# Kernel optimization log

Measured on AMD Instinct MI355X. Metric: run time of the kernel, lower is better.

The kernel has to match this reference:

```python
import jax, jax.numpy as jnp
import numpy as np

EPS = 1e-6


def box2corners(box):
    # box (N,5): x, y, w, h, alpha -> corners (N,4,2), CCW starting at (+w/2,+h/2)
    x, y, w, h, a = (box[:, i] for i in range(5))
    dx = jnp.array([0.5, -0.5, -0.5, 0.5], dtype=box.dtype)
    dy = jnp.array([0.5, 0.5, -0.5, -0.5], dtype=box.dtype)
    cx = dx[None, :] * w[:, None]
    cy = dy[None, :] * h[:, None]
    cos, sin = jnp.cos(a)[:, None], jnp.sin(a)[:, None]
    rx = cx * cos - cy * sin + x[:, None]
    ry = cx * sin + cy * cos + y[:, None]
    return jnp.stack([rx, ry], axis=-1)


def box_intersections(c1, c2):
    # Pairwise intersections of the 4 edges of box1 with the 4 edges of box2.
    # c1, c2: (N,4,2) -> points (N,16,2), valid mask (N,16)
    l1 = jnp.concatenate([c1, jnp.roll(c1, -1, axis=1)], axis=-1)[:, :, None, :]  # (N,4,1,4)
    l2 = jnp.concatenate([c2, jnp.roll(c2, -1, axis=1)], axis=-1)[:, None, :, :]  # (N,1,4,4)
    x1, y1, x2, y2 = (l1[..., i] for i in range(4))
    x3, y3, x4, y4 = (l2[..., i] for i in range(4))
    den = (x2 - x1) * (y4 - y3) - (y2 - y1) * (x4 - x3)
    den_safe = jnp.where(den == 0, 1.0, den)
    t = ((x3 - x1) * (y4 - y3) - (y3 - y1) * (x4 - x3)) / den_safe
    u = ((x3 - x1) * (y2 - y1) - (y3 - y1) * (x2 - x1)) / den_safe
    mask = (den != 0) & (t > 0.0) & (t < 1.0) & (u > 0.0) & (u < 1.0)
    px = x1 + t * (x2 - x1)
    py = y1 + t * (y2 - y1)
    pts = jnp.stack([px, py], axis=-1) * mask[..., None]
    N = c1.shape[0]
    return pts.reshape(N, 16, 2), mask.reshape(N, 16)


def corners_in_box(c1, c2):
    # Which corners of box1 lie inside box2, via projection onto box2 edges. (N,4) bool
    a = c2[:, 0:1]
    ab = c2[:, 1:2] - a
    ad = c2[:, 3:4] - a
    am = c1 - a  # (N,4,2)
    p_ab = (am * ab).sum(-1) / (ab * ab).sum(-1)
    p_ad = (am * ad).sum(-1) / (ad * ad).sum(-1)
    tol = 1e-6
    return (p_ab > -tol) & (p_ab < 1 + tol) & (p_ad > -tol) & (p_ad < 1 + tol)


def sorted_poly_area(pts, mask):
    # Sort valid vertices CCW around the valid-vertex mean, pad invalid slots with the
    # first sorted vertex (degenerate edges contribute 0), then shoelace area.
    # pts (N,M,2), mask (N,M) bool -> area (N,)
    maskf = mask.astype(pts.dtype)
    num = jnp.maximum(maskf.sum(-1, keepdims=True), 1.0)  # avoid /0 for empty polygons
    mean = (pts * maskf[..., None]).sum(1, keepdims=True) / num[..., None]
    centered = pts - mean
    ang = jnp.arctan2(centered[..., 1], centered[..., 0])
    ang = jnp.where(mask, ang, 1e9)  # invalid vertices sort last
    order = jnp.argsort(ang, axis=-1)
    sp = jnp.take_along_axis(pts, order[..., None], axis=1)
    sm = jnp.take_along_axis(mask, order, axis=1)
    sp = jnp.where(sm[..., None], sp, sp[:, 0:1])  # pad with first (valid) vertex
    nxt = jnp.roll(sp, -1, axis=1)
    cross = sp[..., 0] * nxt[..., 1] - sp[..., 1] * nxt[..., 0]
    return jnp.abs(cross.sum(-1)) * 0.5


def intersection_area(c1, c2):
    # Differentiable convex-polygon intersection area (Rotated_IoU style):
    # candidate vertices = corners of each box inside the other + edge intersections.
    ipts, imask = box_intersections(c1, c2)
    m1 = corners_in_box(c1, c2)
    m2 = corners_in_box(c2, c1)
    pts = jnp.concatenate([c1, c2, ipts], axis=1)    # (N,24,2)
    mask = jnp.concatenate([m1, m2, imask], axis=1)  # (N,24)
    return sorted_poly_area(pts, mask)


def poly_giou_loss(pred, target, weight):
    areas1 = pred[:, 2] * pred[:, 3]
    areas2 = target[:, 2] * target[:, 3]
    c1 = box2corners(pred)
    c2 = box2corners(target)
    overlap = intersection_area(c1, c2)
    union = areas1 + areas2 - overlap + EPS
    ious = jnp.maximum(overlap / union, EPS)
    # poly_enclose: all 8 corners, all valid
    all_pts = jnp.concatenate([c1, c2], axis=1)  # (N,8,2)
    enclose = sorted_poly_area(all_pts, jnp.ones(all_pts.shape[:2], bool))
    gious = ious - (enclose - union) / enclose
    loss = 1.0 - gious
    # weighted_loss with reduction='mean', avg_factor=None, loss_weight=1.0
    return (loss * weight).mean()


def setup_inputs() -> dict:
    key = jax.random.key(0)
    k1, k2, k3, k4, k5 = jax.random.split(key, 5)
    N = 500000
    xy = jax.random.uniform(k1, (N, 2), dtype=jnp.float32) * 100.0
    wh = jax.random.uniform(k2, (N, 2), dtype=jnp.float32) * 10.0 + 1.0
    ang = (jax.random.uniform(k3, (N, 1), dtype=jnp.float32) - 0.5) * np.float32(np.pi)
    pred = jnp.concatenate([xy, wh, ang], axis=-1)
    noise = jax.random.normal(k4, (N, 5), dtype=jnp.float32) * jnp.array(
        [1.0, 1.0, 0.5, 0.5, 0.1], dtype=jnp.float32)
    target = pred + noise
    target = target.at[:, 2:4].set(jnp.maximum(target[:, 2:4], 0.5))
    weight = jax.random.uniform(k5, (N,), dtype=jnp.float32)
    return {"pred": pred, "target": target, "weight": weight}


def reference(pred, target, weight):
    return poly_giou_loss(pred, target, weight)
```

## Files before the change

kernel.cpp:

```cpp
#include <hip/hip_runtime.h>
#include <math.h>

#define BLOCK 128
#define NS 8

__device__ __forceinline__ float fast_rcp(float x) {
    return __builtin_amdgcn_rcpf(x);
}

__device__ __forceinline__ float pseudo_angle(float x, float y) {
    float d = fabsf(x) + fabsf(y);
    float p = (d == 0.f) ? 1.f : x * fast_rcp(d);
    return (y < 0.f) ? (p - 1.f) : (1.f - p);
}

__launch_bounds__(BLOCK)
__global__ void giou_kernel(const float* __restrict__ pred,
                            const float* __restrict__ target,
                            const float* __restrict__ weight,
                            float* __restrict__ partials, int N) {
    __shared__ float2 bufA[NS][BLOCK];
    __shared__ float2 bufB[NS][BLOCK];

    int tid = threadIdx.x;
    long gi = (long)blockIdx.x * BLOCK + tid;
    int i = (gi < (long)N) ? (int)gi : (N - 1);

    float p[5], q[5];
#pragma unroll
    for (int j = 0; j < 5; ++j) p[j] = pred[i * 5 + j];
#pragma unroll
    for (int j = 0; j < 5; ++j) q[j] = target[i * 5 + j];
    float wgt = weight[i];

    const float dxs[4] = {0.5f, -0.5f, -0.5f, 0.5f};
    const float dys[4] = {0.5f, 0.5f, -0.5f, -0.5f};
    float c1x[4], c1y[4], c2x[4], c2y[4];
    {
        float sn, cs;
        sincosf(p[4], &sn, &cs);
#pragma unroll
        for (int j = 0; j < 4; ++j) {
            float cx = dxs[j] * p[2], cy = dys[j] * p[3];
            c1x[j] = cx * cs - cy * sn + p[0];
            c1y[j] = cx * sn + cy * cs + p[1];
        }
        sincosf(q[4], &sn, &cs);
#pragma unroll
        for (int j = 0; j < 4; ++j) {
            float cx = dxs[j] * q[2], cy = dys[j] * q[3];
            c2x[j] = cx * cs - cy * sn + q[0];
            c2y[j] = cx * sn + cy * cs + q[1];
        }
    }

    int m1 = 0;
    {
        float e0x = c2x[1] - c2x[0], e0y = c2y[1] - c2y[0];
        float e2x = c2x[3] - c2x[2], e2y = c2y[3] - c2y[2];
        float sA[4], sB[4];
#pragma unroll
        for (int j = 0; j < 4; ++j) {
            sA[j] = e0x * (c1y[j] - c2y[0]) - e0y * (c1x[j] - c2x[0]);
            sB[j] = e2x * (c1y[j] - c2y[2]) - e2y * (c1x[j] - c2x[2]);
        }
#pragma unroll
        for (int e = 0; e < 4; ++e) {
            int en = (e + 1) & 3;
            float cx = c1x[e], cy = c1y[e];
            float dx = c1x[en] - cx, dy = c1y[en] - cy;
            float sac = sA[e], san = sA[en];
            float sbc = sB[e], sbn = sB[en];
            bool inC = (sac >= 0.f) && (sbc >= 0.f);
            bool cA = (sac >= 0.f) != (san >= 0.f);
            bool cB = (sbc >= 0.f) != (sbn >= 0.f);
            float tA = sac * fast_rcp(sac - san);
            float tB = sbc * fast_rcp(sbc - sbn);
            float XAx = fmaf(tA, dx, cx), XAy = fmaf(tA, dy, cy);
            float XBx = fmaf(tB, dx, cx), XBy = fmaf(tB, dy, cy);
            if (inC) { bufA[m1][tid] = make_float2(cx, cy); m1++; }
            bool fA = cA && (!cB || (tA <= tB));
            float X1x = fA ? XAx : XBx, X1y = fA ? XAy : XBy;
            float X2x = fA ? XBx : XAx, X2y = fA ? XBy : XAy;
            if (cA || cB) { bufA[m1][tid] = make_float2(X1x, X1y); m1++; }
            if (cA && cB) { bufA[m1][tid] = make_float2(X2x, X2y); m1++; }
        }
    }
    int n1 = (m1 < 6) ? m1 : 6;

    int m2 = 0;
    {
        float e1x = c2x[2] - c2x[1], e1y = c2y[2] - c2y[1];
        float e3x = c2x[0] - c2x[3], e3y = c2y[0] - c2y[3];
        float vx[6], vy[6], s1[6], s3[6];
#pragma unroll
        for (int j = 0; j < 6; ++j) {
            float2 v = bufA[j][tid];
            vx[j] = v.x; vy[j] = v.y;
            s1[j] = e1x * (v.y - c2y[1]) - e1y * (v.x - c2x[1]);
            s3[j] = e3x * (v.y - c2y[3]) - e3y * (v.x - c2x[3]);
        }
#pragma unroll
        for (int e = 0; e < 6; ++e) {
            bool act = (e < n1);
            bool last = (e == n1 - 1);
            int en = (e + 1 < 6) ? e + 1 : 0;
            float nx = last ? vx[0] : vx[en];
            float ny = last ? vy[0] : vy[en];
            float san = last ? s1[0] : s1[en];
            float sbn = last ? s3[0] : s3[en];
            float cx = vx[e], cy = vy[e];
            float dx = nx - cx, dy = ny - cy;
            float sac = s1[e], sbc = s3[e];
            bool inC = (sac >= 0.f) && (sbc >= 0.f);
            bool cA = (sac >= 0.f) != (san >= 0.f);
            bool cB = (sbc >= 0.f) != (sbn >= 0.f);
            float tA = sac * fast_rcp(sac - san);
            float tB = sbc * fast_rcp(sbc - sbn);
            float XAx = fmaf(tA, dx, cx), XAy = fmaf(tA, dy, cy);
            float XBx = fmaf(tB, dx, cx), XBy = fmaf(tB, dy, cy);
            if (act && inC && m2 < NS) { bufB[m2][tid] = make_float2(cx, cy); m2++; }
            bool fA = cA && (!cB || (tA <= tB));
            float X1x = fA ? XAx : XBx, X1y = fA ? XAy : XBy;
            float X2x = fA ? XBx : XAx, X2y = fA ? XBy : XAy;
            if (act && (cA || cB) && m2 < NS) { bufB[m2][tid] = make_float2(X1x, X1y); m2++; }
            if (act && cA && cB && m2 < NS) { bufB[m2][tid] = make_float2(X2x, X2y); m2++; }
        }
    }
    int n2 = (m2 < NS) ? m2 : NS;

    float overlap;
    {
        float fx[8], fy[8];
#pragma unroll
        for (int k = 0; k < 8; ++k) {
            float2 v = bufB[k][tid];
            fx[k] = v.x; fy[k] = v.y;
        }
#pragma unroll
        for (int k = 1; k < 8; ++k) {
            bool u = (k < n2);
            fx[k] = u ? fx[k] : fx[0];
            fy[k] = u ? fy[k] : fy[0];
        }
        float acc = 0.f;
#pragma unroll
        for (int k = 0; k < 8; ++k) {
            int kn = (k + 1) & 7;
            acc += fx[k] * fy[kn] - fy[k] * fx[kn];
        }
        overlap = 0.5f * fabsf(acc);
        overlap = (n2 >= 3) ? overlap : 0.f;
    }

    float enc;
    {
        float px[8], py[8];
#pragma unroll
        for (int j = 0; j < 4; ++j) {
            px[j] = c1x[j];     py[j] = c1y[j];
            px[4 + j] = c2x[j]; py[4 + j] = c2y[j];
        }
        float ex = 0.f, ey = 0.f;
#pragma unroll
        for (int j = 0; j < 8; ++j) { ex += px[j]; ey += py[j]; }
        float mx = ex * 0.125f, my = ey * 0.125f;
        float ang[8];
#pragma unroll
        for (int j = 0; j < 8; ++j) ang[j] = pseudo_angle(px[j] - mx, py[j] - my);
#pragma unroll
        for (int j = 0; j < 8; ++j) {
            int r = 0;
#pragma unroll
            for (int k = 0; k < 8; ++k) {
                if (k < j)      r += (ang[k] <= ang[j]) ? 1 : 0;
                else if (k > j) r += (ang[k] <  ang[j]) ? 1 : 0;
            }
            bufA[r][tid] = make_float2(px[j], py[j]);
        }
        float sx0[8], sy0[8];
#pragma unroll
        for (int k = 0; k < 8; ++k) {
            float2 v = bufA[k][tid];
            sx0[k] = v.x; sy0[k] = v.y;
        }
        float acc = 0.f;
#pragma unroll
        for (int k = 0; k < 8; ++k) {
            int kn = (k + 1) & 7;
            acc += sx0[k] * sy0[kn] - sy0[k] * sx0[kn];
        }
        enc = 0.5f * fabsf(acc);
    }

    float area1 = p[2] * p[3];
    float area2 = q[2] * q[3];
    float uni = area1 + area2 - overlap + 1e-6f;
    float iou = fmaxf(overlap / uni, 1e-6f);
    float giou = iou - (enc - uni) / enc;
    float loss = (1.f - giou) * wgt;
    if (gi >= (long)N) loss = 0.f;

#pragma unroll
    for (int off = 32; off > 0; off >>= 1)
        loss += __shfl_down(loss, off, 64);
    if ((tid & 63) == 0)
        partials[blockIdx.x * (BLOCK / 64) + (tid >> 6)] = loss;
}

__launch_bounds__(256)
__global__ void reduce_kernel(const float* __restrict__ partials,
                              float* __restrict__ out, int nparts, float scale) {
    __shared__ float acc[4];
    int tid = threadIdx.x;
    float s = 0.f;
    for (int j = tid; j < nparts; j += 256) s += partials[j];
#pragma unroll
    for (int off = 32; off > 0; off >>= 1)
        s += __shfl_down(s, off, 64);
    if ((tid & 63) == 0) acc[tid >> 6] = s;
    __syncthreads();
    if (tid == 0) out[0] = (acc[0] + acc[1] + acc[2] + acc[3]) * scale;
}

extern "C" void kernel_launch(void* const* d_in, const int* in_sizes, int n_in,
                              void* d_out, int out_size, void* d_ws, size_t ws_size,
                              hipStream_t stream) {
    const float* pred   = (const float*)d_in[0];
    const float* target = (const float*)d_in[1];
    const float* weight = (const float*)d_in[2];
    float* out = (float*)d_out;
    float* ws  = (float*)d_ws;
    int N = in_sizes[0] / 5;

    int nblocks = (N + BLOCK - 1) / BLOCK;
    int nparts = nblocks * (BLOCK / 64);
    giou_kernel<<<nblocks, BLOCK, 0, stream>>>(pred, target, weight, ws, N);
    reduce_kernel<<<1, 256, 0, stream>>>(ws, out, nparts, 1.0f / (float)N);
}
```

Baseline: 89.07 us.

## Clip in target's local frame with streaming shoelace, drop LDS clip buffers

The prediction box is transformed into the target box's local frame, where the target is axis-aligned, so Sutherland-Hodgman clipping reduces to comparisons against ±hw and ±hh. Intersection vertices are fed straight into a running shoelace accumulator instead of being written to shared-memory buffers, which removes the bufB array and the intermediate LDS traffic. Accurate sincosf is replaced with the hardware sin/cos builtins, and the final reduction uses 1024 threads instead of 256. The risks are reduced precision from the approximate trig and numerical differences from the changed-frame geometry.

```diff
diff --git a/kernel.cpp b/kernel.cpp
--- a/kernel.cpp
+++ b/kernel.cpp
@@ -2,16 +2,55 @@
 #include <math.h>
 
 #define BLOCK 128
-#define NS 8
 
 __device__ __forceinline__ float fast_rcp(float x) {
     return __builtin_amdgcn_rcpf(x);
+}
+__device__ __forceinline__ float fsin(float x) {
+    return __builtin_amdgcn_sinf(x * 0.15915494309189535f);
+}
+__device__ __forceinline__ float fcos(float x) {
+    return __builtin_amdgcn_cosf(x * 0.15915494309189535f);
 }
 
 __device__ __forceinline__ float pseudo_angle(float x, float y) {
     float d = fabsf(x) + fabsf(y);
     float p = (d == 0.f) ? 1.f : x * fast_rcp(d);
     return (y < 0.f) ? (p - 1.f) : (1.f - p);
+}
+
+struct Shoe {
+    float sfx, sfy, spx, spy, acc;
+    bool have;
+};
+
+__device__ __forceinline__ void emit(Shoe& s, bool c, float X, float Y) {
+    float cr = s.spx * Y - s.spy * X;
+    s.acc += (c && s.have) ? cr : 0.f;
+    s.sfx = (c && !s.have) ? X : s.sfx;
+    s.sfy = (c && !s.have) ? Y : s.sfy;
+    s.spx = c ? X : s.spx;
+    s.spy = c ? Y : s.spy;
+    s.have = s.have || c;
+}
+
+__device__ __forceinline__ void edge_clip_y(Shoe& s, bool en, float ax, float ay,
+                                            float bx, float by, float hh) {
+    bool inA = en && (ay <= hh) && (ay >= -hh);
+    bool cA = en && ((ay > hh) != (by > hh));
+    bool cB = en && ((ay < -hh) != (by < -hh));
+    float dxe = bx - ax, dye = by - ay;
+    float rd = fast_rcp(dye);
+    float tA = (hh - ay) * rd;
+    float tB = (-hh - ay) * rd;
+    float xA = fmaf(tA, dxe, ax);
+    float xB = fmaf(tB, dxe, ax);
+    bool fA = cA && (!cB || (tA <= tB));
+    float e1x = fA ? xA : xB, e1y = fA ? hh : -hh;
+    float e2x = fA ? xB : xA, e2y = fA ? -hh : hh;
+    emit(s, inA, ax, ay);
+    emit(s, cA || cB, e1x, e1y);
+    emit(s, cA && cB, e2x, e2y);
 }
 
 __launch_bounds__(BLOCK)
@@ -19,8 +58,7 @@
                             const float* __restrict__ target,
                             const float* __restrict__ weight,
                             float* __restrict__ partials, int N) {
-    __shared__ float2 bufA[NS][BLOCK];
-    __shared__ float2 bufB[NS][BLOCK];
+    __shared__ float2 bufA[8][BLOCK];
 
     int tid = threadIdx.x;
     long gi = (long)blockIdx.x * BLOCK + tid;
@@ -33,141 +71,83 @@
     for (int j = 0; j < 5; ++j) q[j] = target[i * 5 + j];
     float wgt = weight[i];
 
-    const float dxs[4] = {0.5f, -0.5f, -0.5f, 0.5f};
-    const float dys[4] = {0.5f, 0.5f, -0.5f, -0.5f};
-    float c1x[4], c1y[4], c2x[4], c2y[4];
-    {
-        float sn, cs;
-        sincosf(p[4], &sn, &cs);
-#pragma unroll
-        for (int j = 0; j < 4; ++j) {
-            float cx = dxs[j] * p[2], cy = dys[j] * p[3];
-            c1x[j] = cx * cs - cy * sn + p[0];
-            c1y[j] = cx * sn + cy * cs + p[1];
-        }
-        sincosf(q[4], &sn, &cs);
-#pragma unroll
-        for (int j = 0; j < 4; ++j) {
-            float cx = dxs[j] * q[2], cy = dys[j] * q[3];
-            c2x[j] = cx * cs - cy * sn + q[0];
-            c2y[j] = cx * sn + cy * cs + q[1];
-        }
-    }
-
-    int m1 = 0;
-    {
-        float e0x = c2x[1] - c2x[0], e0y = c2y[1] - c2y[0];
-        float e2x = c2x[3] - c2x[2], e2y = c2y[3] - c2y[2];
-        float sA[4], sB[4];
-#pragma unroll
-        for (int j = 0; j < 4; ++j) {
-            sA[j] = e0x * (c1y[j] - c2y[0]) - e0y * (c1x[j] - c2x[0]);
-            sB[j] = e2x * (c1y[j] - c2y[2]) - e2y * (c1x[j] - c2x[2]);
-        }
-#pragma unroll
-        for (int e = 0; e < 4; ++e) {
-            int en = (e + 1) & 3;
-            float cx = c1x[e], cy = c1y[e];
-            float dx = c1x[en] - cx, dy = c1y[en] - cy;
-            float sac = sA[e], san = sA[en];
-            float sbc = sB[e], sbn = sB[en];
-            bool inC = (sac >= 0.f) && (sbc >= 0.f);
-            bool cA = (sac >= 0.f) != (san >= 0.f);
-            bool cB = (sbc >= 0.f) != (sbn >= 0.f);
-            float tA = sac * fast_rcp(sac - san);
-            float tB = sbc * fast_rcp(sbc - sbn);
-            float XAx = fmaf(tA, dx, cx), XAy = fmaf(tA, dy, cy);
-            float XBx = fmaf(tB, dx, cx), XBy = fmaf(tB, dy, cy);
-            if (inC) { bufA[m1][tid] = make_float2(cx, cy); m1++; }
-            bool fA = cA && (!cB || (tA <= tB));
-            float X1x = fA ? XAx : XBx, X1y = fA ? XAy : XBy;
-            float X2x = fA ? XBx : XAx, X2y = fA ? XBy : XAy;
-            if (cA || cB) { bufA[m1][tid] = make_float2(X1x, X1y); m1++; }
-            if (cA && cB) { bufA[m1][tid] = make_float2(X2x, X2y); m1++; }
-        }
-    }
-    int n1 = (m1 < 6) ? m1 : 6;
-
-    int m2 = 0;
-    {
-        float e1x = c2x[2] - c2x[1], e1y = c2y[2] - c2y[1];
-        float e3x = c2x[0] - c2x[3], e3y = c2y[0] - c2y[3];
-        float vx[6], vy[6], s1[6], s3[6];
-#pragma unroll
-        for (int j = 0; j < 6; ++j) {
-            float2 v = bufA[j][tid];
-            vx[j] = v.x; vy[j] = v.y;
-            s1[j] = e1x * (v.y - c2y[1]) - e1y * (v.x - c2x[1]);
-            s3[j] = e3x * (v.y - c2y[3]) - e3y * (v.x - c2x[3]);
-        }
-#pragma unroll
-        for (int e = 0; e < 6; ++e) {
-            bool act = (e < n1);
-            bool last = (e == n1 - 1);
-            int en = (e + 1 < 6) ? e + 1 : 0;
-            float nx = last ? vx[0] : vx[en];
-            float ny = last ? vy[0] : vy[en];
-            float san = last ? s1[0] : s1[en];
-            float sbn = last ? s3[0] : s3[en];
-            float cx = vx[e], cy = vy[e];
-            float dx = nx - cx, dy = ny - cy;
-            float sac = s1[e], sbc = s3[e];
-            bool inC = (sac >= 0.f) && (sbc >= 0.f);
-            bool cA = (sac >= 0.f) != (san >= 0.f);
-            bool cB = (sbc >= 0.f) != (sbn >= 0.f);
-            float tA = sac * fast_rcp(sac - san);
-            float tB = sbc * fast_rcp(sbc - sbn);
-            float XAx = fmaf(tA, dx, cx), XAy = fmaf(tA, dy, cy);
-            float XBx = fmaf(tB, dx, cx), XBy = fmaf(tB, dy, cy);
-            if (act && inC && m2 < NS) { bufB[m2][tid] = make_float2(cx, cy); m2++; }
-            bool fA = cA && (!cB || (tA <= tB));
-            float X1x = fA ? XAx : XBx, X1y = fA ? XAy : XBy;
-            float X2x = fA ? XBx : XAx, X2y = fA ? XBy : XAy;
-            if (act && (cA || cB) && m2 < NS) { bufB[m2][tid] = make_float2(X1x, X1y); m2++; }
-            if (act && cA && cB && m2 < NS) { bufB[m2][tid] = make_float2(X2x, X2y); m2++; }
-        }
-    }
-    int n2 = (m2 < NS) ? m2 : NS;
-
-    float overlap;
-    {
-        float fx[8], fy[8];
-#pragma unroll
-        for (int k = 0; k < 8; ++k) {
-            float2 v = bufB[k][tid];
-            fx[k] = v.x; fy[k] = v.y;
-        }
-#pragma unroll
-        for (int k = 1; k < 8; ++k) {
-            bool u = (k < n2);
-            fx[k] = u ? fx[k] : fx[0];
-            fy[k] = u ? fy[k] : fy[0];
-        }
-        float acc = 0.f;
-#pragma unroll
-        for (int k = 0; k < 8; ++k) {
-            int kn = (k + 1) & 7;
-            acc += fx[k] * fy[kn] - fy[k] * fx[kn];
-        }
-        overlap = 0.5f * fabsf(acc);
-        overlap = (n2 >= 3) ? overlap : 0.f;
-    }
+    float cq = fcos(q[4]), sq = fsin(q[4]);
+    float dang = p[4] - q[4];
+    float cd = fcos(dang), sd = fsin(dang);
+    float hw = 0.5f * q[2], hh = 0.5f * q[3];
+    float dxc = p[0] - q[0], dyc = p[1] - q[1];
+    float tx = dxc * cq + dyc * sq;
+    float ty = -dxc * sq + dyc * cq;
+    float ax_ = 0.5f * p[2] * cd, ay_ = 0.5f * p[2] * sd;
+    float bx_ = -0.5f * p[3] * sd, by_ = 0.5f * p[3] * cd;
+
+    float qx[4], qy[4];
+    qx[0] = tx + ax_ + bx_; qy[0] = ty + ay_ + by_;
+    qx[1] = tx - ax_ + bx_; qy[1] = ty - ay_ + by_;
+    qx[2] = tx - ax_ - bx_; qy[2] = ty - ay_ - by_;
+    qx[3] = tx + ax_ - bx_; qy[3] = ty + ay_ - by_;
+
+    float sxk[8], syk[8];
+    bool sv[8];
+#pragma unroll
+    for (int e = 0; e < 4; ++e) {
+        int en = (e + 1) & 3;
+        float xc = qx[e], yc = qy[e], xn = qx[en], yn = qy[en];
+        float dxe = xn - xc, dye = yn - yc;
+        bool inC = (xc <= hw) && (xc >= -hw);
+        bool cA = (xc > hw) != (xn > hw);
+        bool cB = (xc < -hw) != (xn < -hw);
+        float rd = fast_rcp(dxe);
+        float tA = (hw - xc) * rd;
+        float tB = (-hw - xc) * rd;
+        float yA = fmaf(tA, dye, yc);
+        float yB = fmaf(tB, dye, yc);
+        bool fA = cA && (!cB || (tA <= tB));
+        float X1x = fA ? hw : -hw, X1y = fA ? yA : yB;
+        float X2x = fA ? -hw : hw, X2y = fA ? yB : yA;
+        sxk[2 * e]     = inC ? xc : X1x;
+        syk[2 * e]     = inC ? yc : X1y;
+        sv[2 * e]      = inC || cA || cB;
+        sxk[2 * e + 1] = inC ? X1x : X2x;
+        syk[2 * e + 1] = inC ? X1y : X2y;
+        sv[2 * e + 1]  = inC ? (cA || cB) : (cA && cB);
+    }
+
+    Shoe sh; sh.sfx = sh.sfy = sh.spx = sh.spy = sh.acc = 0.f; sh.have = false;
+    bool have_p = false;
+    float pfx = 0.f, pfy = 0.f, pvx = 0.f, pvy = 0.f;
+#pragma unroll
+    for (int k = 0; k < 8; ++k) {
+        bool val = sv[k];
+        float cx_ = sxk[k], cy_ = syk[k];
+        edge_clip_y(sh, have_p && val, pvx, pvy, cx_, cy_, hh);
+        pfx = (val && !have_p) ? cx_ : pfx;
+        pfy = (val && !have_p) ? cy_ : pfy;
+        pvx = val ? cx_ : pvx;
+        pvy = val ? cy_ : pvy;
+        have_p = have_p || val;
+    }
+    edge_clip_y(sh, have_p, pvx, pvy, pfx, pfy, hh);
+    float wrap = sh.spx * sh.sfy - sh.spy * sh.sfx;
+    float accs = sh.acc + (sh.have ? wrap : 0.f);
+    float overlap = 0.5f * fabsf(accs);
 
     float enc;
     {
-        float px[8], py[8];
-#pragma unroll
-        for (int j = 0; j < 4; ++j) {
-            px[j] = c1x[j];     py[j] = c1y[j];
-            px[4 + j] = c2x[j]; py[4 + j] = c2y[j];
-        }
+        float px8[8], py8[8];
+#pragma unroll
+        for (int j = 0; j < 4; ++j) { px8[j] = qx[j]; py8[j] = qy[j]; }
+        px8[4] = hw;  py8[4] = hh;
+        px8[5] = -hw; py8[5] = hh;
+        px8[6] = -hw; py8[6] = -hh;
+        px8[7] = hw;  py8[7] = -hh;
         float ex = 0.f, ey = 0.f;
 #pragma unroll
-        for (int j = 0; j < 8; ++j) { ex += px[j]; ey += py[j]; }
+        for (int j = 0; j < 8; ++j) { ex += px8[j]; ey += py8[j]; }
         float mx = ex * 0.125f, my = ey * 0.125f;
         float ang[8];
 #pragma unroll
-        for (int j = 0; j < 8; ++j) ang[j] = pseudo_angle(px[j] - mx, py[j] - my);
+        for (int j = 0; j < 8; ++j) ang[j] = pseudo_angle(px8[j] - mx, py8[j] - my);
 #pragma unroll
         for (int j = 0; j < 8; ++j) {
             int r = 0;
@@ -176,7 +156,7 @@
                 if (k < j)      r += (ang[k] <= ang[j]) ? 1 : 0;
                 else if (k > j) r += (ang[k] <  ang[j]) ? 1 : 0;
             }
-            bufA[r][tid] = make_float2(px[j], py[j]);
+            bufA[r][tid] = make_float2(px8[j], py8[j]);
         }
         float sx0[8], sy0[8];
 #pragma unroll
@@ -184,13 +164,13 @@
             float2 v = bufA[k][tid];
             sx0[k] = v.x; sy0[k] = v.y;
         }
-        float acc = 0.f;
+        float acc2 = 0.f;
 #pragma unroll
         for (int k = 0; k < 8; ++k) {
             int kn = (k + 1) & 7;
-            acc += sx0[k] * sy0[kn] - sy0[k] * sx0[kn];
+            acc2 += sx0[k] * sy0[kn] - sy0[k] * sx0[kn];
         }
-        enc = 0.5f * fabsf(acc);
+        enc = 0.5f * fabsf(acc2);
     }
 
     float area1 = p[2] * p[3];
@@ -208,19 +188,24 @@
         partials[blockIdx.x * (BLOCK / 64) + (tid >> 6)] = loss;
 }
 
-__launch_bounds__(256)
+__launch_bounds__(1024)
 __global__ void reduce_kernel(const float* __restrict__ partials,
                               float* __restrict__ out, int nparts, float scale) {
-    __shared__ float acc[4];
+    __shared__ float acc[16];
     int tid = threadIdx.x;
     float s = 0.f;
-    for (int j = tid; j < nparts; j += 256) s += partials[j];
+    for (int j = tid; j < nparts; j += 1024) s += partials[j];
 #pragma unroll
     for (int off = 32; off > 0; off >>= 1)
         s += __shfl_down(s, off, 64);
     if ((tid & 63) == 0) acc[tid >> 6] = s;
     __syncthreads();
-    if (tid == 0) out[0] = (acc[0] + acc[1] + acc[2] + acc[3]) * scale;
+    if (tid == 0) {
+        float t = 0.f;
+#pragma unroll
+        for (int k = 0; k < 16; ++k) t += acc[k];
+        out[0] = t * scale;
+    }
 }
 
 extern "C" void kernel_launch(void* const* d_in, const int* in_sizes, int n_in,
@@ -236,5 +221,5 @@
     int nblocks = (N + BLOCK - 1) / BLOCK;
     int nparts = nblocks * (BLOCK / 64);
     giou_kernel<<<nblocks, BLOCK, 0, stream>>>(pred, target, weight, ws, N);
-    reduce_kernel<<<1, 256, 0, stream>>>(ws, out, nparts, 1.0f / (float)N);
-}
+    reduce_kernel<<<1, 1024, 0, stream>>>(ws, out, nparts, 1.0f / (float)N);
+}
```

New measurement: 80.59 us. -9.5%, faster.
